# Performance work log

Measured on AMD Instinct MI355X. Metric: run time of the kernel, lower is better.

Reference implementation:

```python
import jax, jax.numpy as jnp
import numpy as np

N = 100_000      # nodes
E = 400_000      # edges
POS = 3          # pos_dim
F = 128          # feats_dim (kernel_dim)
M = 16           # m_dim
FE = 16          # fourier_features
EIN = 2 * F + 2 * FE + 1   # 289 edge mlp input
EHID = 2 * EIN             # 578
NIN = F + M                # 144
NHID = 2 * F               # 256
EPS = 1e-5


def _ln(x, g, b):
    m = x.mean(-1, keepdims=True)
    v = ((x - m) ** 2).mean(-1, keepdims=True)
    return (x - m) * jax.lax.rsqrt(v + EPS) * g + b


def setup_inputs() -> dict:
    key = jax.random.key(0)
    ks = jax.random.split(key, 8)

    def xav(k, i, o):
        return jax.random.normal(k, (i, o), jnp.float32) * np.float32(np.sqrt(2.0 / (i + o)))

    x = jax.random.normal(ks[0], (N, POS + F), jnp.float32)
    edge_index = jax.random.randint(ks[1], (2, E), 0, N, dtype=jnp.int64)
    return {
        "x": x,
        "edge_index": edge_index,
        "e_w1": xav(ks[2], EIN, EHID), "e_b1": jnp.zeros((EHID,), jnp.float32),
        "e_w2": xav(ks[3], EHID, M),   "e_b2": jnp.zeros((M,), jnp.float32),
        "en1_g": jnp.ones((M,), jnp.float32), "en1_b": jnp.zeros((M,), jnp.float32),
        "en2_g": jnp.ones((M,), jnp.float32), "en2_b": jnp.zeros((M,), jnp.float32),
        "nn1_g": jnp.ones((F,), jnp.float32), "nn1_b": jnp.zeros((F,), jnp.float32),
        "n_w1": xav(ks[4], NIN, NHID), "n_b1": jnp.zeros((NHID,), jnp.float32),
        "n_w2": xav(ks[5], NHID, F),   "n_b2": jnp.zeros((F,), jnp.float32),
        "nn2_g": jnp.ones((F,), jnp.float32), "nn2_b": jnp.zeros((F,), jnp.float32),
    }


def reference(x, edge_index, e_w1, e_b1, e_w2, e_b2, en1_g, en1_b, en2_g, en2_b,
              nn1_g, nn1_b, n_w1, n_b1, n_w2, n_b2, nn2_g, nn2_b):
    coors, feats = x[:, :POS], x[:, POS:]
    src, dst = edge_index[0], edge_index[1]  # x_j = feats[src], x_i = feats[dst]

    rel = coors[src] - coors[dst]                      # [E,3]
    d = (rel ** 2).sum(-1, keepdims=True)              # [E,1] squared distance
    scales = jnp.asarray(2.0, jnp.float32) ** jnp.arange(FE)
    ds = d / scales                                    # [E,FE]
    edge_attr = jnp.concatenate([jnp.sin(ds), jnp.cos(ds), d], -1)  # [E,2*FE+1]

    # edge MLP + LayerNorm (message)
    m = jnp.concatenate([feats[dst], feats[src], edge_attr], -1)    # [E,EIN]
    m = jax.nn.silu(m @ e_w1 + e_b1)
    m = jax.nn.silu(m @ e_w2 + e_b2)                                # [E,M]
    m = _ln(m, en1_g, en1_b)

    # scatter-add to target nodes, then LayerNorm
    m_i = jax.ops.segment_sum(m, dst, num_segments=N)               # [N,M]
    m_i = _ln(m_i, en2_g, en2_b)

    # node update MLP with residual
    h = jnp.concatenate([_ln(feats, nn1_g, nn1_b), m_i], -1)        # [N,NIN]
    h = jax.nn.silu(h @ n_w1 + n_b1)
    h = h @ n_w2 + n_b2
    h = _ln(h, nn2_g, nn2_b)
    out = feats + h
    return jnp.concatenate([coors, out], -1)                        # [N,POS+F]
```

## Files before the change

kernel.cpp:

```cpp
#include <hip/hip_runtime.h>
#include <math.h>

#define N_NODES 100000
#define N_EDGES 400000
#define POSD 3
#define F 128
#define M 16
#define EIN 289
#define EHID 578
#define NIN 144
#define NHID 256
#define ROW 131
#define LNEPS 1e-5f

#define KP 320
#define KPA 328
#define NP 640
#define EPB 32
#define NSLICE 10
#define NTW 5
#define HIDP 640
#define HIDPA 648

#define NPB2 80
#define NK1P 168
#define NSL2 5
#define NHIDP 264

#define PSTR 584
#define ARBF_STR 72
#define PPB 32

#define WS_W1KS   6400000
#define WS_W2T    6809600
#define WS_FEATS  6830080
#define WS_W1KS2  32430080
#define WS_W2KS   32512000
#define WS_B1H    32577536
#define WS_PD     33554432LL
#define WS_PS     (WS_PD + 116800000LL + 4096LL)
#define WS_FAST_NEED (WS_PS + 116800000LL + 4096LL)

typedef _Float16 half8 __attribute__((ext_vector_type(8)));
typedef _Float16 half4 __attribute__((ext_vector_type(4)));
typedef float f32x4 __attribute__((ext_vector_type(4)));

__device__ __forceinline__ float silu_f(float v) {
    return v * __builtin_amdgcn_rcpf(1.f + __expf(-v));
}

__global__ __launch_bounds__(256) void prep_feats(
    const float* __restrict__ x, _Float16* __restrict__ feats)
{
    long long i = (long long)blockIdx.x * 256 + threadIdx.x;
    if (i < (long long)N_NODES * F) {
        int n = (int)(i >> 7), k = (int)(i & 127);
        feats[i] = (_Float16)x[(long long)n * ROW + POSD + k];
    }
}

__global__ __launch_bounds__(256) void prep_weights(
    const float* __restrict__ w1, const float* __restrict__ w2,
    const float* __restrict__ b1,
    _Float16* __restrict__ w1ks, _Float16* __restrict__ w2t,
    _Float16* __restrict__ b1h)
{
    long long idx = (long long)blockIdx.x * 256 + threadIdx.x;
    const long long n1 = (long long)NSLICE * NP * 32;
    const long long n2 = n1 + (long long)M * HIDP;
    if (idx < n1) {
        int s   = (int)(idx / (NP * 32));
        int rem = (int)(idx - (long long)s * (NP * 32));
        int c   = rem >> 5;
        int kk  = rem & 31;
        int k   = s * 32 + kk;
        float v = (k < EIN && c < EHID) ? w1[(long long)k * EHID + c] : 0.f;
        w1ks[idx] = (_Float16)v;
    } else if (idx < n2) {
        long long j = idx - n1;
        int oc = (int)(j / HIDP);
        int k  = (int)(j - (long long)oc * HIDP);
        float v = (k < EHID) ? w2[(long long)k * M + oc] : 0.f;
        w2t[j] = (_Float16)v;
    } else if (idx < n2 + HIDP) {
        int j = (int)(idx - n2);
        b1h[j] = (_Float16)((j < EHID) ? b1[j] : 0.f);
    }
}

__global__ __launch_bounds__(256) void prep_weights_node(
    const float* __restrict__ w1, const float* __restrict__ w2,
    _Float16* __restrict__ w1ks2, _Float16* __restrict__ w2ks)
{
    int idx = blockIdx.x * 256 + threadIdx.x;
    const int n1 = NSL2 * 256 * 32;
    if (idx < n1) {
        int s = idx >> 13, rem = idx & 8191;
        int c = rem >> 5, kk = rem & 31;
        int k = s * 32 + kk;
        w1ks2[idx] = (_Float16)((k < NIN) ? w1[k * NHID + c] : 0.f);
    } else if (idx < n1 + 8 * 128 * 32) {
        int j = idx - n1;
        int s = j >> 12, rem = j & 4095;
        int c = rem >> 5, kk = rem & 31;
        int k = s * 32 + kk;
        w2ks[j] = (_Float16)w2[k * F + c];
    }
}

__global__ __launch_bounds__(512, 2) void prep_pdps(
    const _Float16* __restrict__ feats, const _Float16* __restrict__ w1ks,
    _Float16* __restrict__ Pd, _Float16* __restrict__ Ps)
{
    __shared__ __align__(16) _Float16 st[2][PPB][PSTR];
    const int t = threadIdx.x;
    const int lane = t & 63, wv = t >> 6, cl16 = lane & 15, h4 = lane >> 4;
    const long long nb = (long long)blockIdx.x * PPB;
    const bool live[5] = {
        (wv * 5 + 0) * 16 < EHID, (wv * 5 + 1) * 16 < EHID,
        (wv * 5 + 2) * 16 < EHID, (wv * 5 + 3) * 16 < EHID,
        (wv * 5 + 4) * 16 < EHID };

    f32x4 acc[2][2][5] = {};
    #pragma unroll
    for (int s = 0; s < 4; ++s) {
        half8 bf[2][5];
        #pragma unroll
        for (int hf = 0; hf < 2; ++hf)
            #pragma unroll
            for (int nt = 0; nt < 5; ++nt)
                if (live[nt])
                    bf[hf][nt] = *(const half8*)(w1ks + (long long)(hf * 4 + s) * (NP * 32)
                                                 + (wv * 5 + nt) * 512 + cl16 * 32 + h4 * 8);
        half8 af[2];
        #pragma unroll
        for (int mt = 0; mt < 2; ++mt)
            af[mt] = *(const half8*)(feats + (nb + mt * 16 + cl16) * F + s * 32 + h4 * 8);
        #pragma unroll
        for (int hf = 0; hf < 2; ++hf)
            #pragma unroll
            for (int nt = 0; nt < 5; ++nt)
                if (live[nt]) {
                    #pragma unroll
                    for (int mt = 0; mt < 2; ++mt)
                        acc[hf][mt][nt] = __builtin_amdgcn_mfma_f32_16x16x32_f16(
                                              af[mt], bf[hf][nt], acc[hf][mt][nt], 0, 0, 0);
                }
    }

    #pragma unroll
    for (int hf = 0; hf < 2; ++hf) {
        #pragma unroll
        for (int nt = 0; nt < 5; ++nt) {
            if (!live[nt]) continue;
            int hcol = (wv * 5 + nt) * 16 + cl16;
            if (hcol < PSTR) {
                #pragma unroll
                for (int mt = 0; mt < 2; ++mt) {
                    #pragma unroll
                    for (int r = 0; r < 4; ++r)
                        st[hf][mt * 16 + h4 * 4 + r][hcol] = (_Float16)acc[hf][mt][nt][r];
                }
            }
        }
    }
    __syncthreads();

    const int row = t >> 4;
    const int gw  = t & 15;
    #pragma unroll
    for (int k = 0; k < 5; ++k) {
        int g = gw + 16 * k;
        if (g < PSTR / 8) {
            *(half8*)(Pd + (nb + row) * PSTR + g * 8) = *(const half8*)(&st[0][row][g * 8]);
            *(half8*)(Ps + (nb + row) * PSTR + g * 8) = *(const half8*)(&st[1][row][g * 8]);
        }
    }
}

__global__ __launch_bounds__(512, 4) void edge_fast(
    const float* __restrict__ x, const int* __restrict__ ei,
    const _Float16* __restrict__ w1ks, const _Float16* __restrict__ b1h,
    const _Float16* __restrict__ w2t, const float* __restrict__ b2,
    const float* __restrict__ g1, const float* __restrict__ bb1,
    float* __restrict__ m_i,
    const _Float16* __restrict__ Pd, const _Float16* __restrict__ Ps)
{
    __shared__ __align__(16) _Float16 lds_H[EPB * HIDPA];
    __shared__ __align__(16) char ubuf[8192];
    __shared__ int   src_s[EPB], dst_s[EPB];
    __shared__ float d_s[EPB];
    _Float16* A_rbf = (_Float16*)ubuf;
    float (*part)[EPB][M] = (float (*)[EPB][M])ubuf;

    const int t    = threadIdx.x;
    const int lane = t & 63;
    const int wv   = t >> 6;
    const int cl16 = lane & 15;
    const int h4   = lane >> 4;
    const long long ebase = (long long)blockIdx.x * EPB;

    if (t < EPB) {
        int s = ei[ebase + t];
        int d = ei[(long long)N_EDGES + ebase + t];
        src_s[t] = s; dst_s[t] = d;
        float dx = x[(long long)s*ROW+0] - x[(long long)d*ROW+0];
        float dy = x[(long long)s*ROW+1] - x[(long long)d*ROW+1];
        float dz = x[(long long)s*ROW+2] - x[(long long)d*ROW+2];
        d_s[t] = dx*dx + dy*dy + dz*dz;
    }
    __syncthreads();

    for (int i = t; i < EPB * 64; i += 512) {
        int row = i >> 6, j = i & 63;
        float dv = d_s[row];
        float ds = ldexpf(dv, -(j & 15));
        float v = (j < 16) ? __sinf(ds) : (j < 32) ? __cosf(ds)
                : (j == 32) ? dv : 0.f;
        A_rbf[row * ARBF_STR + j] = (_Float16)v;
    }
    __syncthreads();

    f32x4 acc[2][NTW] = {};
    const bool live[NTW] = {
        (wv * NTW + 0) * 16 < EHID, (wv * NTW + 1) * 16 < EHID,
        (wv * NTW + 2) * 16 < EHID, (wv * NTW + 3) * 16 < EHID,
        (wv * NTW + 4) * 16 < EHID };
    #pragma unroll
    for (int s = 0; s < 2; ++s) {
        half8 bf[NTW];
        #pragma unroll
        for (int nt = 0; nt < NTW; ++nt)
            if (live[nt])
                bf[nt] = *(const half8*)(w1ks + (long long)(8 + s) * (NP * 32)
                                         + (wv * NTW + nt) * 512 + cl16 * 32 + h4 * 8);
        #pragma unroll
        for (int mt = 0; mt < 2; ++mt) {
            const half8 af = *(const half8*)(A_rbf + (mt * 16 + cl16) * ARBF_STR
                                             + s * 32 + h4 * 8);
            #pragma unroll
            for (int nt = 0; nt < NTW; ++nt)
                if (live[nt])
                    acc[mt][nt] = __builtin_amdgcn_mfma_f32_16x16x32_f16(
                                      af, bf[nt], acc[mt][nt], 0, 0, 0);
        }
    }

    const int ce = t >> 4;
    const int g0 = t & 15;
    const long long pdrow = (long long)dst_s[ce] * PSTR;
    const long long psrow = (long long)src_s[ce] * PSTR;
    half8 pd8[5], ps8[5];
    #pragma unroll
    for (int p = 0; p < 5; ++p) {
        int g = g0 + 16 * p;
        if (g < PSTR / 8) {
            pd8[p] = *(const half8*)(Pd + pdrow + g * 8);
            ps8[p] = *(const half8*)(Ps + psrow + g * 8);
        } else {
            pd8[p] = (half8)(_Float16)0.f;
            ps8[p] = (half8)(_Float16)0.f;
        }
    }
    half8 bq[5];
    {
        const int kq = wv >> 1;
        #pragma unroll
        for (int k5 = 0; k5 < 5; ++k5)
            bq[k5] = *(const half8*)(w2t + cl16 * HIDP + (kq * 5 + k5) * 32 + h4 * 8);
    }

    #pragma unroll
    for (int nt = 0; nt < NTW; ++nt) {
        if (!live[nt]) continue;
        int hcol = (wv * NTW + nt) * 16 + cl16;
        #pragma unroll
        for (int mt = 0; mt < 2; ++mt) {
            #pragma unroll
            for (int r = 0; r < 4; ++r) {
                int edge = mt * 16 + h4 * 4 + r;
                lds_H[edge * HIDPA + hcol] = (_Float16)acc[mt][nt][r];
            }
        }
    }
    __syncthreads();

    #pragma unroll
    for (int p = 0; p < 5; ++p) {
        int g = g0 + 16 * p;
        half8 rb = *(const half8*)(lds_H + ce * HIDPA + g * 8);
        half8 bb = *(const half8*)(b1h + g * 8);
        half8 sum = pd8[p] + ps8[p] + rb + bb;
        half8 o;
        #pragma unroll
        for (int j = 0; j < 8; ++j) {
            int h = g * 8 + j;
            float v = (float)sum[j];
            o[j] = (h < EHID) ? (_Float16)silu_f(v) : (_Float16)0.f;
        }
        *(half8*)(lds_H + ce * HIDPA + g * 8) = o;
    }
    __syncthreads();

    {
        const int eh = wv & 1;
        const int kq = wv >> 1;
        f32x4 acc2 = {};
        const int oc = cl16;
        const int edgeA = eh * 16 + oc;
        #pragma unroll
        for (int k5 = 0; k5 < 5; ++k5) {
            int G2 = (kq * 5 + k5) * 4 + h4;
            const half8 a = *(const half8*)(lds_H + edgeA * HIDPA + G2 * 8);
            acc2 = __builtin_amdgcn_mfma_f32_16x16x32_f16(a, bq[k5], acc2, 0, 0, 0);
        }
        #pragma unroll
        for (int r = 0; r < 4; ++r)
            part[kq][eh * 16 + h4 * 4 + r][cl16] = acc2[r];
    }
    __syncthreads();

    if (wv < 2) {
        const int eh = wv;
        const int oc = cl16;
        float g = g1[oc], bb = bb1[oc], b2v = b2[oc];
        #pragma unroll
        for (int r = 0; r < 4; ++r) {
            int edge = eh * 16 + h4 * 4 + r;
            float v = part[0][edge][oc] + part[1][edge][oc]
                    + part[2][edge][oc] + part[3][edge][oc] + b2v;
            v = silu_f(v);
            float s = v, s2 = v * v;
            #pragma unroll
            for (int m = 8; m >= 1; m >>= 1) {
                s  += __shfl_xor(s,  m, 16);
                s2 += __shfl_xor(s2, m, 16);
            }
            float mean = s * (1.f / 16.f);
            float var  = s2 * (1.f / 16.f) - mean * mean;
            float outv = (v - mean) * rsqrtf(var + LNEPS) * g + bb;
            atomicAdd(&m_i[(long long)dst_s[edge] * M + oc], outv);
        }
    }
}

__global__ __launch_bounds__(512, 4) void edge_fused(
    const _Float16* __restrict__ feats, const float* __restrict__ x,
    const int* __restrict__ ei,
    const _Float16* __restrict__ w1ks, const float* __restrict__ b1,
    const _Float16* __restrict__ w2t, const float* __restrict__ b2,
    const float* __restrict__ g1, const float* __restrict__ bb1,
    float* __restrict__ m_i)
{
    __shared__ __align__(16) _Float16 smem[EPB * HIDPA];
    _Float16* lds_A = smem;
    _Float16* lds_H = smem;
    __shared__ float part[4][EPB][M];
    __shared__ int   src_s[EPB], dst_s[EPB];
    __shared__ float d_s[EPB];

    const int t    = threadIdx.x;
    const int lane = t & 63;
    const int wv   = t >> 6;
    const int cl16 = lane & 15;
    const int h4   = lane >> 4;
    const long long ebase = (long long)blockIdx.x * EPB;

    if (t < EPB) {
        int s = ei[ebase + t];
        int d = ei[(long long)N_EDGES + ebase + t];
        src_s[t] = s; dst_s[t] = d;
        float dx = x[(long long)s*ROW+0] - x[(long long)d*ROW+0];
        float dy = x[(long long)s*ROW+1] - x[(long long)d*ROW+1];
        float dz = x[(long long)s*ROW+2] - x[(long long)d*ROW+2];
        d_s[t] = dx*dx + dy*dy + dz*dz;
    }
    __syncthreads();

    for (int i = t; i < EPB * 32; i += 512) {
        int row = i >> 5, g = i & 31;
        int node = (g < 16) ? dst_s[row] : src_s[row];
        half8 v = *(const half8*)(feats + (long long)node * F + ((g & 15) << 3));
        *(half8*)(lds_A + row * KPA + (g << 3)) = v;
    }
    for (int i = t; i < EPB * 64; i += 512) {
        int row = i >> 6, j = i & 63;
        float dv = d_s[row];
        float ds = ldexpf(dv, -(j & 15));
        float v = (j < 16) ? __sinf(ds) : (j < 32) ? __cosf(ds)
                : (j == 32) ? dv : 0.f;
        lds_A[row * KPA + 256 + j] = (_Float16)v;
    }
    __syncthreads();

    f32x4 acc[2][NTW] = {};
    const bool live[NTW] = {
        (wv * NTW + 0) * 16 < EHID, (wv * NTW + 1) * 16 < EHID,
        (wv * NTW + 2) * 16 < EHID, (wv * NTW + 3) * 16 < EHID,
        (wv * NTW + 4) * 16 < EHID };
    #pragma unroll
    for (int s = 0; s < NSLICE; ++s) {
        half8 bf[NTW];
        #pragma unroll
        for (int nt = 0; nt < NTW; ++nt)
            if (live[nt])
                bf[nt] = *(const half8*)(w1ks + (long long)s * (NP * 32)
                                         + (wv * NTW + nt) * 512 + cl16 * 32 + h4 * 8);
        const int G = s * 4 + h4;
        half8 af[2];
        #pragma unroll
        for (int mt = 0; mt < 2; ++mt)
            af[mt] = *(const half8*)(lds_A + (mt * 16 + cl16) * KPA + G * 8);
        #pragma unroll
        for (int nt = 0; nt < NTW; ++nt)
            if (live[nt]) {
                #pragma unroll
                for (int mt = 0; mt < 2; ++mt)
                    acc[mt][nt] = __builtin_amdgcn_mfma_f32_16x16x32_f16(
                                      af[mt], bf[nt], acc[mt][nt], 0, 0, 0);
            }
    }

    half8 bq[5];
    {
        const int kq = wv >> 1;
        #pragma unroll
        for (int k5 = 0; k5 < 5; ++k5)
            bq[k5] = *(const half8*)(w2t + cl16 * HIDP + (kq * 5 + k5) * 32 + h4 * 8);
    }
    __syncthreads();

    #pragma unroll
    for (int nt = 0; nt < NTW; ++nt) {
        int hcol = (wv * NTW + nt) * 16 + cl16;
        float bias = (hcol < EHID) ? b1[hcol] : 0.f;
        #pragma unroll
        for (int mt = 0; mt < 2; ++mt) {
            #pragma unroll
            for (int r = 0; r < 4; ++r) {
                int edge = mt * 16 + h4 * 4 + r;
                float v = (hcol < EHID) ? silu_f(acc[mt][nt][r] + bias) : 0.f;
                lds_H[edge * HIDPA + hcol] = (_Float16)v;
            }
        }
    }
    __syncthreads();

    {
        const int eh = wv & 1;
        const int kq = wv >> 1;
        f32x4 acc2 = {};
        const int oc = cl16;
        const int edgeA = eh * 16 + oc;
        #pragma unroll
        for (int k5 = 0; k5 < 5; ++k5) {
            int G2 = (kq * 5 + k5) * 4 + h4;
            const half8 a = *(const half8*)(lds_H + edgeA * HIDPA + G2 * 8);
            acc2 = __builtin_amdgcn_mfma_f32_16x16x32_f16(a, bq[k5], acc2, 0, 0, 0);
        }
        #pragma unroll
        for (int r = 0; r < 4; ++r)
            part[kq][eh * 16 + h4 * 4 + r][oc] = acc2[r];
    }
    __syncthreads();

    if (wv < 2) {
        const int eh = wv;
        const int oc = cl16;
        float g = g1[oc], bb = bb1[oc], b2v = b2[oc];
        #pragma unroll
        for (int r = 0; r < 4; ++r) {
            int edge = eh * 16 + h4 * 4 + r;
            float v = part[0][edge][oc] + part[1][edge][oc]
                    + part[2][edge][oc] + part[3][edge][oc] + b2v;
            v = silu_f(v);
            float s = v, s2 = v * v;
            #pragma unroll
            for (int m = 8; m >= 1; m >>= 1) {
                s  += __shfl_xor(s,  m, 16);
                s2 += __shfl_xor(s2, m, 16);
            }
            float mean = s * (1.f / 16.f);
            float var  = s2 * (1.f / 16.f) - mean * mean;
            float outv = (v - mean) * rsqrtf(var + LNEPS) * g + bb;
            atomicAdd(&m_i[(long long)dst_s[edge] * M + oc], outv);
        }
    }
}

__global__ __launch_bounds__(512, 4) void node_kernel(
    const _Float16* __restrict__ feats, const float* __restrict__ x,
    const float* __restrict__ m_i,
    const float* __restrict__ en2g, const float* __restrict__ en2b,
    const float* __restrict__ nn1g, const float* __restrict__ nn1b,
    const _Float16* __restrict__ w1ks2, const float* __restrict__ b1,
    const _Float16* __restrict__ w2ks, const float* __restrict__ b2,
    const float* __restrict__ nn2g, const float* __restrict__ nn2b,
    float* __restrict__ out)
{
    __shared__ __align__(16) _Float16 smem[NPB2 * NHIDP];
    _Float16* lds_A = smem;
    _Float16* lds_H = smem;
    __shared__ float rsum2[NPB2], rsq2[NPB2];

    const int t    = threadIdx.x;
    const int lane = t & 63;
    const int wv   = t >> 6;
    const int cl16 = lane & 15;
    const int h4   = lane >> 4;
    const long long nb = (long long)blockIdx.x * NPB2;

    if (t < NPB2) { rsum2[t] = 0.f; rsq2[t] = 0.f; }

    #pragma unroll
    for (int p = 0; p < 5; ++p) {
        int nl = p * 16 + (t >> 5);
        int l  = t & 31;
        half4 v4 = *(const half4*)(feats + (nb + nl) * F + l * 4);
        float v[4]; float s = 0.f, s2 = 0.f;
        #pragma unroll
        for (int i = 0; i < 4; ++i) {
            v[i] = (float)v4[i]; s += v[i]; s2 += v[i]*v[i];
        }
        #pragma unroll
        for (int m = 16; m >= 1; m >>= 1) {
            s  += __shfl_xor(s,  m, 32);
            s2 += __shfl_xor(s2, m, 32);
        }
        float mean = s * (1.f/128.f);
        float var  = s2 * (1.f/128.f) - mean*mean;
        float rs   = rsqrtf(var + LNEPS);
        half4 w;
        #pragma unroll
        for (int i = 0; i < 4; ++i) {
            int c = l * 4 + i;
            w[i] = (_Float16)((v[i] - mean) * rs * nn1g[c] + nn1b[c]);
        }
        *(half4*)(lds_A + nl * NK1P + l * 4) = w;
    }
    for (int i = t; i < NPB2 * M; i += 512) {
        int nl = i >> 4, oc = i & 15;
        float v = m_i[(nb + nl) * M + oc];
        float a = v, a2 = v * v;
        #pragma unroll
        for (int m = 8; m >= 1; m >>= 1) {
            a  += __shfl_xor(a,  m, 16);
            a2 += __shfl_xor(a2, m, 16);
        }
        float mn = a * (1.f/16.f);
        float vr = a2 * (1.f/16.f) - mn*mn;
        float lv = (v - mn) * rsqrtf(vr + LNEPS) * en2g[oc] + en2b[oc];
        lds_A[nl * NK1P + 128 + oc] = (_Float16)lv;
    }
    for (int i = t; i < NPB2 * 16; i += 512) {
        int nl = i >> 4, j = i & 15;
        lds_A[nl * NK1P + 144 + j] = (_Float16)0.f;
    }
    __syncthreads();

    f32x4 acc[5][2] = {};
    #pragma unroll
    for (int s = 0; s < NSL2; ++s) {
        half8 bf[2];
        #pragma unroll
        for (int nt = 0; nt < 2; ++nt)
            bf[nt] = *(const half8*)(w1ks2 + s * (NHID * 32)
                                     + (wv * 2 + nt) * 512 + cl16 * 32 + h4 * 8);
        const int G = s * 4 + h4;
        half8 af[5];
        #pragma unroll
        for (int mt = 0; mt < 5; ++mt)
            af[mt] = *(const half8*)(lds_A + (mt * 16 + cl16) * NK1P + G * 8);
        #pragma unroll
        for (int nt = 0; nt < 2; ++nt) {
            #pragma unroll
            for (int mt = 0; mt < 5; ++mt)
                acc[mt][nt] = __builtin_amdgcn_mfma_f32_16x16x32_f16(
                                  af[mt], bf[nt], acc[mt][nt], 0, 0, 0);
        }
    }
    __syncthreads();

    #pragma unroll
    for (int nt = 0; nt < 2; ++nt) {
        int hcol = (wv * 2 + nt) * 16 + cl16;
        float bias = b1[hcol];
        #pragma unroll
        for (int mt = 0; mt < 5; ++mt) {
            #pragma unroll
            for (int r = 0; r < 4; ++r) {
                int row = mt * 16 + h4 * 4 + r;
                float v = silu_f(acc[mt][nt][r] + bias);
                lds_H[row * NHIDP + hcol] = (_Float16)v;
            }
        }
    }
    __syncthreads();

    f32x4 acc2[5] = {};
    const int col = wv * 16 + cl16;
    #pragma unroll
    for (int s = 0; s < 8; ++s) {
        const half8 b = *(const half8*)(w2ks + s * (F * 32) + col * 32 + h4 * 8);
        const int G2 = s * 4 + h4;
        #pragma unroll
        for (int mt = 0; mt < 5; ++mt) {
            int row = mt * 16 + cl16;
            const half8 a = *(const half8*)(lds_H + row * NHIDP + G2 * 8);
            acc2[mt] = __builtin_amdgcn_mfma_f32_16x16x32_f16(a, b, acc2[mt], 0, 0, 0);
        }
    }

    float y[5][4];
    float b2v = b2[col];
    #pragma unroll
    for (int mt = 0; mt < 5; ++mt) {
        #pragma unroll
        for (int r = 0; r < 4; ++r) {
            float v = acc2[mt][r] + b2v;
            y[mt][r] = v;
            float s = v, s2 = v * v;
            #pragma unroll
            for (int m = 8; m >= 1; m >>= 1) {
                s  += __shfl_xor(s,  m, 16);
                s2 += __shfl_xor(s2, m, 16);
            }
            if (cl16 == 0) {
                int row = mt * 16 + h4 * 4 + r;
                atomicAdd(&rsum2[row], s);
                atomicAdd(&rsq2[row],  s2);
            }
        }
    }
    __syncthreads();

    float gcol2 = nn2g[col], bcol2 = nn2b[col];
    #pragma unroll
    for (int mt = 0; mt < 5; ++mt) {
        #pragma unroll
        for (int r = 0; r < 4; ++r) {
            int row = mt * 16 + h4 * 4 + r;
            long long node = nb + row;
            float mn = rsum2[row] * (1.f/128.f);
            float vr = rsq2[row] * (1.f/128.f) - mn*mn;
            float rs = rsqrtf(vr + LNEPS);
            float res = x[node * ROW + POSD + col];
            out[node * ROW + POSD + col] = res + (y[mt][r] - mn) * rs * gcol2 + bcol2;
        }
    }
    for (int i = t; i < NPB2 * POSD; i += 512) {
        int nl = i / 3, c = i - nl * 3;
        long long node = nb + nl;
        out[node * ROW + c] = x[node * ROW + c];
    }
}

extern "C" void kernel_launch(void* const* d_in, const int* in_sizes, int n_in,
                              void* d_out, int out_size, void* d_ws, size_t ws_size,
                              hipStream_t stream) {
    const float* x    = (const float*)d_in[0];
    const int*   ei   = (const int*)d_in[1];
    const float* e_w1 = (const float*)d_in[2];
    const float* e_b1 = (const float*)d_in[3];
    const float* e_w2 = (const float*)d_in[4];
    const float* e_b2 = (const float*)d_in[5];
    const float* en1g = (const float*)d_in[6];
    const float* en1b = (const float*)d_in[7];
    const float* en2g = (const float*)d_in[8];
    const float* en2b = (const float*)d_in[9];
    const float* nn1g = (const float*)d_in[10];
    const float* nn1b = (const float*)d_in[11];
    const float* n_w1 = (const float*)d_in[12];
    const float* n_b1 = (const float*)d_in[13];
    const float* n_w2 = (const float*)d_in[14];
    const float* n_b2 = (const float*)d_in[15];
    const float* nn2g = (const float*)d_in[16];
    const float* nn2b = (const float*)d_in[17];
    float* out = (float*)d_out;

    char* ws = (char*)d_ws;
    float*    m_i   = (float*)ws;
    _Float16* w1ks  = (_Float16*)(ws + WS_W1KS);
    _Float16* w2t   = (_Float16*)(ws + WS_W2T);
    _Float16* feats = (_Float16*)(ws + WS_FEATS);
    _Float16* w1ks2 = (_Float16*)(ws + WS_W1KS2);
    _Float16* w2ks  = (_Float16*)(ws + WS_W2KS);
    _Float16* b1h   = (_Float16*)(ws + WS_B1H);
    _Float16* Pd    = (_Float16*)(ws + WS_PD);
    _Float16* Ps    = (_Float16*)(ws + WS_PS);

    const bool fast = ws_size >= (size_t)WS_FAST_NEED;

    hipMemsetAsync(m_i, 0, (size_t)N_NODES * M * sizeof(float), stream);
    prep_weights<<<843, 256, 0, stream>>>(e_w1, e_w2, e_b1, w1ks, w2t, b1h);
    prep_weights_node<<<288, 256, 0, stream>>>(n_w1, n_w2, w1ks2, w2ks);
    prep_feats<<<(N_NODES * F + 255) / 256, 256, 0, stream>>>(x, feats);

    if (fast) {
        prep_pdps<<<N_NODES / PPB, 512, 0, stream>>>(feats, w1ks, Pd, Ps);
        edge_fast<<<N_EDGES / EPB, 512, 0, stream>>>(
            x, ei, w1ks, b1h, w2t, e_b2, en1g, en1b, m_i, Pd, Ps);
    } else {
        edge_fused<<<N_EDGES / EPB, 512, 0, stream>>>(
            feats, x, ei, w1ks, e_b1, w2t, e_b2, en1g, en1b, m_i);
    }
    node_kernel<<<N_NODES / NPB2, 512, 0, stream>>>(
        feats, x, m_i, en2g, en2b, nn1g, nn1b, w1ks2, n_b1, w2ks, n_b2, nn2g, nn2b, out);
}
```

Measured before the change: 502.4 us.

## Bucket-sort edges by destination before the fused edge kernel

```diff
diff --git a/kernel.cpp b/kernel.cpp
--- a/kernel.cpp
+++ b/kernel.cpp
@@ -30,6 +30,7 @@
 #define PSTR 584
 #define ARBF_STR 72
 #define PPB 32
+#define NBUCK 3125
 
 #define WS_W1KS   6400000
 #define WS_W2T    6809600
@@ -39,7 +40,10 @@
 #define WS_B1H    32577536
 #define WS_PD     33554432LL
 #define WS_PS     (WS_PD + 116800000LL + 4096LL)
-#define WS_FAST_NEED (WS_PS + 116800000LL + 4096LL)
+#define WS_SORTED (WS_PS + 116800000LL + 4096LL)
+#define WS_BCNT   (WS_SORTED + 1600000LL)
+#define WS_BOFF   (WS_BCNT + 16384LL)
+#define WS_FAST_NEED (WS_BOFF + 16384LL)
 
 typedef _Float16 half8 __attribute__((ext_vector_type(8)));
 typedef _Float16 half4 __attribute__((ext_vector_type(4)));
@@ -108,6 +112,51 @@
     }
 }
 
+__global__ __launch_bounds__(256) void bucket_hist(
+    const int* __restrict__ ei, int* __restrict__ cnt)
+{
+    int e = blockIdx.x * 256 + threadIdx.x;
+    if (e < N_EDGES) atomicAdd(&cnt[ei[N_EDGES + e] >> 5], 1);
+}
+
+__global__ __launch_bounds__(1024) void bucket_scan(
+    const int* __restrict__ cnt, int* __restrict__ off)
+{
+    __shared__ int smem[1024];
+    __shared__ int running;
+    const int t = threadIdx.x;
+    if (t == 0) running = 0;
+    __syncthreads();
+    for (int base = 0; base < NBUCK; base += 1024) {
+        int i = base + t;
+        int v = (i < NBUCK) ? cnt[i] : 0;
+        smem[t] = v;
+        __syncthreads();
+        #pragma unroll
+        for (int ofs = 1; ofs < 1024; ofs <<= 1) {
+            int add = (t >= ofs) ? smem[t - ofs] : 0;
+            __syncthreads();
+            smem[t] += add;
+            __syncthreads();
+        }
+        int excl = smem[t] - v + running;
+        if (i < NBUCK) off[i] = excl;
+        __syncthreads();
+        if (t == 0) running += smem[1023];
+        __syncthreads();
+    }
+}
+
+__global__ __launch_bounds__(256) void bucket_scatter(
+    const int* __restrict__ ei, int* __restrict__ off, int* __restrict__ sorted)
+{
+    int e = blockIdx.x * 256 + threadIdx.x;
+    if (e < N_EDGES) {
+        int slot = atomicAdd(&off[ei[N_EDGES + e] >> 5], 1);
+        sorted[slot] = e;
+    }
+}
+
 __global__ __launch_bounds__(512, 2) void prep_pdps(
     const _Float16* __restrict__ feats, const _Float16* __restrict__ w1ks,
     _Float16* __restrict__ Pd, _Float16* __restrict__ Ps)
@@ -180,6 +229,7 @@
 
 __global__ __launch_bounds__(512, 4) void edge_fast(
     const float* __restrict__ x, const int* __restrict__ ei,
+    const int* __restrict__ sorted,
     const _Float16* __restrict__ w1ks, const _Float16* __restrict__ b1h,
     const _Float16* __restrict__ w2t, const float* __restrict__ b2,
     const float* __restrict__ g1, const float* __restrict__ bb1,
@@ -201,8 +251,9 @@
     const long long ebase = (long long)blockIdx.x * EPB;
 
     if (t < EPB) {
-        int s = ei[ebase + t];
-        int d = ei[(long long)N_EDGES + ebase + t];
+        int e = sorted[ebase + t];
+        int s = ei[e];
+        int d = ei[(long long)N_EDGES + e];
         src_s[t] = s; dst_s[t] = d;
         float dx = x[(long long)s*ROW+0] - x[(long long)d*ROW+0];
         float dy = x[(long long)s*ROW+1] - x[(long long)d*ROW+1];
@@ -679,15 +730,18 @@
     float* out = (float*)d_out;
 
     char* ws = (char*)d_ws;
-    float*    m_i   = (float*)ws;
-    _Float16* w1ks  = (_Float16*)(ws + WS_W1KS);
-    _Float16* w2t   = (_Float16*)(ws + WS_W2T);
-    _Float16* feats = (_Float16*)(ws + WS_FEATS);
-    _Float16* w1ks2 = (_Float16*)(ws + WS_W1KS2);
-    _Float16* w2ks  = (_Float16*)(ws + WS_W2KS);
-    _Float16* b1h   = (_Float16*)(ws + WS_B1H);
-    _Float16* Pd    = (_Float16*)(ws + WS_PD);
-    _Float16* Ps    = (_Float16*)(ws + WS_PS);
+    float*    m_i    = (float*)ws;
+    _Float16* w1ks   = (_Float16*)(ws + WS_W1KS);
+    _Float16* w2t    = (_Float16*)(ws + WS_W2T);
+    _Float16* feats  = (_Float16*)(ws + WS_FEATS);
+    _Float16* w1ks2  = (_Float16*)(ws + WS_W1KS2);
+    _Float16* w2ks   = (_Float16*)(ws + WS_W2KS);
+    _Float16* b1h    = (_Float16*)(ws + WS_B1H);
+    _Float16* Pd     = (_Float16*)(ws + WS_PD);
+    _Float16* Ps     = (_Float16*)(ws + WS_PS);
+    int*      sorted = (int*)(ws + WS_SORTED);
+    int*      bcnt   = (int*)(ws + WS_BCNT);
+    int*      boff   = (int*)(ws + WS_BOFF);
 
     const bool fast = ws_size >= (size_t)WS_FAST_NEED;
 
@@ -697,9 +751,13 @@
     prep_feats<<<(N_NODES * F + 255) / 256, 256, 0, stream>>>(x, feats);
 
     if (fast) {
+        hipMemsetAsync(bcnt, 0, NBUCK * sizeof(int), stream);
+        bucket_hist<<<(N_EDGES + 255) / 256, 256, 0, stream>>>(ei, bcnt);
+        bucket_scan<<<1, 1024, 0, stream>>>(bcnt, boff);
+        bucket_scatter<<<(N_EDGES + 255) / 256, 256, 0, stream>>>(ei, boff, sorted);
         prep_pdps<<<N_NODES / PPB, 512, 0, stream>>>(feats, w1ks, Pd, Ps);
         edge_fast<<<N_EDGES / EPB, 512, 0, stream>>>(
-            x, ei, w1ks, b1h, w2t, e_b2, en1g, en1b, m_i, Pd, Ps);
+            x, ei, sorted, w1ks, b1h, w2t, e_b2, en1g, en1b, m_i, Pd, Ps);
     } else {
         edge_fused<<<N_EDGES / EPB, 512, 0, stream>>>(
             feats, x, ei, w1ks, e_b1, w2t, e_b2, en1g, en1b, m_i);
```

Result: faster. 489.7 us (-2.5%).
